# Optimization experiments

Measured on AMD Instinct MI355X. Metric: run time of the kernel, lower is better.

## Reference

```python
import jax, jax.numpy as jnp
import numpy as np

B, D, E, H, O, TOP_K = 65536, 256, 16, 256, 256, 2
GATE_T = 1.0  # gate_temperature default


def setup_inputs() -> dict:
    key = jax.random.key(0)
    ks = jax.random.split(key, 8)
    sn = lambda k, shape, sc: (jax.random.normal(k, shape, jnp.float32) * sc)
    return {
        "x": sn(ks[0], (B, D), 1.0),
        # per-expert input bias, init N(0, 0.02) as in the module
        "bias": sn(ks[1], (E, D), 0.02),
        # expert MLP params: Linear(D,H) -> ReLU -> Linear(H,O), stacked over experts
        "W1": sn(ks[2], (E, D, H), 1.0 / np.sqrt(D)),
        "b1": jnp.zeros((E, H), jnp.float32),
        "W2": sn(ks[3], (E, H, O), 1.0 / np.sqrt(H)),
        "b2": jnp.zeros((E, O), jnp.float32),
        # gate MLP: Linear(D,4D) -> ReLU -> Linear(4D,D) -> ReLU -> Linear(D,E)
        "g1": sn(ks[4], (D, 4 * D), 1.0 / np.sqrt(D)),
        "gb1": jnp.zeros((4 * D,), jnp.float32),
        "g2": sn(ks[5], (4 * D, D), 1.0 / np.sqrt(4 * D)),
        "gb2": jnp.zeros((D,), jnp.float32),
        "g3": sn(ks[6], (D, E), 1.0 / np.sqrt(D)),
        "gb3": jnp.zeros((E,), jnp.float32),
    }


def reference(x, bias, W1, b1, W2, b2, g1, gb1, g2, gb2, g3, gb3):
    # --- gate ---
    h = jax.nn.relu(x @ g1 + gb1)
    h = jax.nn.relu(h @ g2 + gb2)
    gate_logits = h @ g3 + gb3              # [B, E]
    T = max(GATE_T, 1e-6)
    p = jax.nn.softmax(gate_logits / T, axis=1)

    # --- top-k sparsification + renormalize (top_k < num_experts) ---
    topv, topi = jax.lax.top_k(p, TOP_K)    # [B, K]
    rows = jnp.arange(p.shape[0])[:, None]
    p_sparse = jnp.zeros_like(p).at[rows, topi].set(topv)
    p = p_sparse / (p_sparse.sum(axis=1, keepdims=True) + 1e-9)

    # --- dense all-experts compute (module runs every expert on every token) ---
    xb = x[:, None, :] + bias[None]                                  # [B, E, D]
    he = jax.nn.relu(jnp.einsum("bed,edh->beh", xb, W1) + b1)      # [B, E, H]
    outs_all = jnp.einsum("beh,eho->beo", he, W2) + b2             # [B, E, O]

    # --- weighted combine (stopgrad_gate=False -> grads flow through p) ---
    y = jnp.einsum("be,beo->bo", p, outs_all)                      # [B, O]
    return (y, p)
```

## Files before the change

kernel.cpp:

```cpp
#include <hip/hip_runtime.h>
#include <cstdint>
#include <cstddef>

#define BTOK 65536
#define DDIM 256
#define NEXP 16
#define HDIM 256
#define ODIM 256
#define TAU2 1.2e-2f
#define TAU3 1.2e-4
#define AMB2_CAP 12288
#define AMB3_CAP 1024

typedef _Float16 fp16x8 __attribute__((ext_vector_type(8)));
typedef float    f32x4_t __attribute__((ext_vector_type(4)));

__device__ __forceinline__ void async_ld16(const void* g, void* l) {
  __builtin_amdgcn_global_load_lds(
      (const __attribute__((address_space(1))) unsigned int*)g,
      (__attribute__((address_space(3))) unsigned int*)l, 16, 0, 0);
}

__global__ __launch_bounds__(256) void k_transpose_cvt(
    const float* __restrict__ src, _Float16* __restrict__ dhi,
    _Float16* __restrict__ dlo, int R, int C) {
  __shared__ float s[32][33];
  int bz = blockIdx.z;
  size_t stride = (size_t)R * C;
  src += (size_t)bz * stride;
  dhi += (size_t)bz * stride;
  if (dlo) dlo += (size_t)bz * stride;
  int c0 = blockIdx.x * 32, r0 = blockIdx.y * 32;
  int tx = threadIdx.x & 31, ty = threadIdx.x >> 5;
  for (int k = 0; k < 32; k += 8)
    s[ty + k][tx] = src[(size_t)(r0 + ty + k) * C + c0 + tx];
  __syncthreads();
  for (int k = 0; k < 32; k += 8) {
    float v = s[tx][ty + k];
    _Float16 h = (_Float16)v;
    size_t o = (size_t)(c0 + ty + k) * R + r0 + tx;
    dhi[o] = h;
    if (dlo) dlo[o] = (_Float16)(v - (float)h);
  }
}

__global__ __launch_bounds__(256) void k_xcvt_hi(const float* __restrict__ x,
                                                 _Float16* __restrict__ xhi, int n8) {
  int i = blockIdx.x * 256 + threadIdx.x;
  if (i >= n8) return;
  const float4* p = (const float4*)x;
  float4 a = p[(size_t)i * 2], b = p[(size_t)i * 2 + 1];
  float v[8] = {a.x, a.y, a.z, a.w, b.x, b.y, b.z, b.w};
  fp16x8 hv;
#pragma unroll
  for (int j = 0; j < 8; j++) hv[j] = (_Float16)v[j];
  *(fp16x8*)(xhi + (size_t)i * 8) = hv;
}

__global__ __launch_bounds__(256) void k_gemm_f16(
    const _Float16* __restrict__ A, const _Float16* __restrict__ B,
    const float* __restrict__ bias, _Float16* __restrict__ C,
    int M, int N, int K) {
  __shared__ _Float16 sA[128 * 32], sB[128 * 32];
  const int tid = threadIdx.x;
  const int lane = tid & 63;
  const int wave = tid >> 6;
  const int wr = wave >> 1, wc = wave & 1;
  const int m0 = blockIdx.y * 128, n0 = blockIdx.x * 128;
  f32x4_t zero4 = {0.f, 0.f, 0.f, 0.f};
  f32x4_t acc[4][4];
#pragma unroll
  for (int i = 0; i < 4; i++)
#pragma unroll
    for (int j = 0; j < 4; j++) acc[i][j] = zero4;

  for (int k0 = 0; k0 < K; k0 += 32) {
#pragma unroll
    for (int r = 0; r < 2; r++) {
      int idx = r * 256 + tid;
      int row = idx >> 2, ch = idx & 3;
      int gch = ch ^ (row & 3);
      async_ld16(A + (size_t)(m0 + row) * K + k0 + gch * 8, &sA[idx * 8]);
      async_ld16(B + (size_t)(n0 + row) * K + k0 + gch * 8, &sB[idx * 8]);
    }
    __syncthreads();
    fp16x8 a[4], b[4];
    int kc = lane >> 4;
#pragma unroll
    for (int i = 0; i < 4; i++) {
      int ar = wr * 64 + i * 16 + (lane & 15);
      a[i] = *(const fp16x8*)&sA[ar * 32 + ((kc ^ (ar & 3)) << 3)];
      int br = wc * 64 + i * 16 + (lane & 15);
      b[i] = *(const fp16x8*)&sB[br * 32 + ((kc ^ (br & 3)) << 3)];
    }
#pragma unroll
    for (int i = 0; i < 4; i++)
#pragma unroll
      for (int j = 0; j < 4; j++)
        acc[i][j] = __builtin_amdgcn_mfma_f32_16x16x32_f16(a[i], b[j], acc[i][j], 0, 0, 0);
    __syncthreads();
  }
#pragma unroll
  for (int j = 0; j < 4; j++) {
    int col = n0 + wc * 64 + j * 16 + (lane & 15);
    float bc = bias[col];
#pragma unroll
    for (int i = 0; i < 4; i++)
#pragma unroll
      for (int q = 0; q < 4; q++) {
        int row = m0 + wr * 64 + i * 16 + ((lane >> 4) << 2) + q;
        float v = acc[i][j][q] + bc;
        v = v > 0.f ? v : 0.f;
        C[(size_t)row * N + col] = (_Float16)v;
      }
  }
}

__global__ __launch_bounds__(256) void k_gemm_split(
    const _Float16* __restrict__ Ahi, const _Float16* __restrict__ Alo,
    const _Float16* __restrict__ Bhi, const _Float16* __restrict__ Blo,
    const float* __restrict__ bias,
    _Float16* __restrict__ Chi, _Float16* __restrict__ Clo,
    int M, int N, int K, const int* __restrict__ nAct) {
  int nA = *nAct;
  if (nA > M) nA = M;
  const int m0 = blockIdx.y * 128, n0 = blockIdx.x * 128;
  if (m0 >= nA) return;
  __shared__ _Float16 sAh[128 * 32], sAl[128 * 32], sBh[128 * 32], sBl[128 * 32];
  const int tid = threadIdx.x;
  const int lane = tid & 63;
  const int wave = tid >> 6;
  const int wr = wave >> 1, wc = wave & 1;
  f32x4_t zero4 = {0.f, 0.f, 0.f, 0.f};
  f32x4_t acc[4][4];
#pragma unroll
  for (int i = 0; i < 4; i++)
#pragma unroll
    for (int j = 0; j < 4; j++) acc[i][j] = zero4;

  for (int k0 = 0; k0 < K; k0 += 32) {
#pragma unroll
    for (int r = 0; r < 2; r++) {
      int idx = r * 256 + tid;
      int row = idx >> 2, ch = idx & 3;
      int gch = ch ^ (row & 3);
      size_t ga = (size_t)(m0 + row) * K + k0 + gch * 8;
      size_t gb = (size_t)(n0 + row) * K + k0 + gch * 8;
      async_ld16(Ahi + ga, &sAh[idx * 8]);
      async_ld16(Alo + ga, &sAl[idx * 8]);
      async_ld16(Bhi + gb, &sBh[idx * 8]);
      async_ld16(Blo + gb, &sBl[idx * 8]);
    }
    __syncthreads();
    fp16x8 ah[4], al[4], bh[4], bl[4];
    int kc = lane >> 4;
#pragma unroll
    for (int i = 0; i < 4; i++) {
      int ar = wr * 64 + i * 16 + (lane & 15);
      int offa = ar * 32 + ((kc ^ (ar & 3)) << 3);
      ah[i] = *(const fp16x8*)&sAh[offa];
      al[i] = *(const fp16x8*)&sAl[offa];
      int br = wc * 64 + i * 16 + (lane & 15);
      int offb = br * 32 + ((kc ^ (br & 3)) << 3);
      bh[i] = *(const fp16x8*)&sBh[offb];
      bl[i] = *(const fp16x8*)&sBl[offb];
    }
#pragma unroll
    for (int i = 0; i < 4; i++)
#pragma unroll
      for (int j = 0; j < 4; j++) {
        acc[i][j] = __builtin_amdgcn_mfma_f32_16x16x32_f16(ah[i], bh[j], acc[i][j], 0, 0, 0);
        acc[i][j] = __builtin_amdgcn_mfma_f32_16x16x32_f16(ah[i], bl[j], acc[i][j], 0, 0, 0);
        acc[i][j] = __builtin_amdgcn_mfma_f32_16x16x32_f16(al[i], bh[j], acc[i][j], 0, 0, 0);
      }
    __syncthreads();
  }
#pragma unroll
  for (int j = 0; j < 4; j++) {
    int col = n0 + wc * 64 + j * 16 + (lane & 15);
    float bc = bias[col];
#pragma unroll
    for (int i = 0; i < 4; i++)
#pragma unroll
      for (int q = 0; q < 4; q++) {
        int row = m0 + wr * 64 + i * 16 + ((lane >> 4) << 2) + q;
        float v = acc[i][j][q] + bc;
        v = v > 0.f ? v : 0.f;
        _Float16 h = (_Float16)v;
        size_t o = (size_t)row * N + col;
        Chi[o] = h;
        Clo[o] = (_Float16)(v - (float)h);
      }
  }
}

__global__ __launch_bounds__(256) void k_gate3_fast(
    const _Float16* __restrict__ h2h, const float* __restrict__ g3,
    const float* __restrict__ gb3,
    float* __restrict__ pout, int* __restrict__ idx0, int* __restrict__ idx1,
    float* __restrict__ w0, float* __restrict__ w1,
    int* __restrict__ amb2Cnt, int* __restrict__ amb2List,
    int* __restrict__ cnt0, int* __restrict__ cnt1) {
  __shared__ _Float16 shh[16 * 256];
  __shared__ float sg3[16][260];
  __shared__ float sgb[16];
  __shared__ float slog[16][17];
  __shared__ int sidx[16][2];
  __shared__ float swv[16][2];
  __shared__ int hc0[16], hc1[16];
  int tid = threadIdx.x;
  int tokBase = blockIdx.x * 16;
  if (tid < 16) { hc0[tid] = 0; hc1[tid] = 0; }
  {
    int t = tid >> 4, c = (tid & 15) * 16;
    size_t g = (size_t)(tokBase + t) * 256 + c;
    *(fp16x8*)&shh[t * 256 + c] = *(const fp16x8*)&h2h[g];
    *(fp16x8*)&shh[t * 256 + c + 8] = *(const fp16x8*)&h2h[g + 8];
  }
#pragma unroll
  for (int r = 0; r < 16; r++) {
    int j = r * 256 + tid;
    sg3[j & 15][j >> 4] = g3[j];
  }
  if (tid < 16) sgb[tid] = gb3[tid];
  __syncthreads();
  int t = tid >> 4, e = tid & 15;
  const _Float16* ph = &shh[t * 256];
  const float* pg = &sg3[e][0];
  float acc = 0.f;
  for (int k = 0; k < 256; k += 8) {
    fp16x8 hv = *(const fp16x8*)&ph[k];
    float4 ga = *(const float4*)&pg[k];
    float4 gb = *(const float4*)&pg[k + 4];
    acc = fmaf((float)hv[0], ga.x, acc);
    acc = fmaf((float)hv[1], ga.y, acc);
    acc = fmaf((float)hv[2], ga.z, acc);
    acc = fmaf((float)hv[3], ga.w, acc);
    acc = fmaf((float)hv[4], gb.x, acc);
    acc = fmaf((float)hv[5], gb.y, acc);
    acc = fmaf((float)hv[6], gb.z, acc);
    acc = fmaf((float)hv[7], gb.w, acc);
  }
  acc += sgb[e];
  slog[t][e] = acc;
  __syncthreads();
  if (e == 0) {
    float l[16];
#pragma unroll
    for (int i = 0; i < 16; i++) l[i] = slog[t][i];
    int i1 = 0;
    for (int i = 1; i < 16; i++) if (l[i] > l[i1]) i1 = i;
    int i2 = -1;
    for (int i = 0; i < 16; i++) { if (i == i1) continue; if (i2 < 0 || l[i] > l[i2]) i2 = i; }
    float l3 = -1e30f;
    for (int i = 0; i < 16; i++) { if (i == i1 || i == i2) continue; if (l[i] > l3) l3 = l[i]; }
    float lmax = l[i1];
    float S = 0.f;
    for (int i = 0; i < 16; i++) S += expf(l[i] - lmax);
    float p1 = 1.0f / S, p2 = expf(l[i2] - lmax) / S;
    float den = p1 + p2 + 1e-9f;
    sidx[t][0] = i1; sidx[t][1] = i2;
    swv[t][0] = p1 / den; swv[t][1] = p2 / den;
    atomicAdd(&hc0[i1], 1);
    atomicAdd(&hc1[i2], 1);
    if (l[i2] - l3 < TAU2) {
      int pos = atomicAdd(amb2Cnt, 1);
      if (pos < AMB2_CAP) amb2List[pos] = tokBase + t;
    }
  }
  __syncthreads();
  int i1 = sidx[t][0], i2 = sidx[t][1];
  float pv = (e == i1) ? swv[t][0] : ((e == i2) ? swv[t][1] : 0.f);
  pout[(size_t)(tokBase + t) * 16 + e] = pv;
  if (e == 0) {
    int tok = tokBase + t;
    idx0[tok] = i1; idx1[tok] = i2;
    w0[tok] = swv[t][0]; w1[tok] = swv[t][1];
  }
  if (tid < 16) {
    if (hc0[tid]) atomicAdd(&cnt0[tid], hc0[tid]);
    if (hc1[tid]) atomicAdd(&cnt1[tid], hc1[tid]);
  }
}

__global__ __launch_bounds__(256) void k_gather2(
    const float* __restrict__ x, const int* __restrict__ cnt,
    const int* __restrict__ list,
    _Float16* __restrict__ xgh, _Float16* __restrict__ xgl) {
  int n = *cnt; if (n > AMB2_CAP) n = AMB2_CAP;
  int s = blockIdx.x * 8 + (threadIdx.x >> 5);
  if (s >= n) return;
  int tok = list[s];
  int c = (threadIdx.x & 31) * 8;
  const float4* p = (const float4*)&x[(size_t)tok * 256 + c];
  float4 a = p[0], b = p[1];
  float v[8] = {a.x, a.y, a.z, a.w, b.x, b.y, b.z, b.w};
  fp16x8 hv, lv;
#pragma unroll
  for (int j = 0; j < 8; j++) {
    _Float16 h = (_Float16)v[j];
    hv[j] = h;
    lv[j] = (_Float16)(v[j] - (float)h);
  }
  *(fp16x8*)&xgh[(size_t)s * 256 + c] = hv;
  *(fp16x8*)&xgl[(size_t)s * 256 + c] = lv;
}

__global__ __launch_bounds__(256) void k_gate3_precise(
    const _Float16* __restrict__ h2ghi, const _Float16* __restrict__ h2glo,
    const float* __restrict__ g3, const float* __restrict__ gb3,
    const int* __restrict__ amb2Cnt, const int* __restrict__ amb2List,
    float* __restrict__ pout, int* __restrict__ idx0, int* __restrict__ idx1,
    float* __restrict__ w0, float* __restrict__ w1,
    int* __restrict__ amb3Cnt, int* __restrict__ amb3List,
    int* __restrict__ cnt0, int* __restrict__ cnt1) {
  __shared__ _Float16 shh[16 * 256], shl[16 * 256];
  __shared__ float sg3[16][260];
  __shared__ float sgb[16];
  __shared__ double slog[16][17];
  __shared__ int sidx[16][2];
  __shared__ float swv[16][2];
  int tid = threadIdx.x;
  int slotBase = blockIdx.x * 16;
  int n2 = *amb2Cnt; if (n2 > AMB2_CAP) n2 = AMB2_CAP;
  {
    int t = tid >> 4, c = (tid & 15) * 16;
    size_t g = (size_t)(slotBase + t) * 256 + c;
    *(fp16x8*)&shh[t * 256 + c] = *(const fp16x8*)&h2ghi[g];
    *(fp16x8*)&shh[t * 256 + c + 8] = *(const fp16x8*)&h2ghi[g + 8];
    *(fp16x8*)&shl[t * 256 + c] = *(const fp16x8*)&h2glo[g];
    *(fp16x8*)&shl[t * 256 + c + 8] = *(const fp16x8*)&h2glo[g + 8];
  }
#pragma unroll
  for (int r = 0; r < 16; r++) {
    int j = r * 256 + tid;
    sg3[j & 15][j >> 4] = g3[j];
  }
  if (tid < 16) sgb[tid] = gb3[tid];
  __syncthreads();
  int t = tid >> 4, e = tid & 15;
  int slot = slotBase + t;
  const _Float16* ph = &shh[t * 256];
  const _Float16* pl = &shl[t * 256];
  const float* pg = &sg3[e][0];
  double acc = 0.0;
  for (int k = 0; k < 256; k += 4) {
#pragma unroll
    for (int j = 0; j < 4; j++) {
      double a = (double)(float)ph[k + j] + (double)(float)pl[k + j];
      acc = fma(a, (double)pg[k + j], acc);
    }
  }
  acc += (double)sgb[e];
  slog[t][e] = acc;
  __syncthreads();
  if (e == 0 && slot < n2) {
    int tok = amb2List[slot];
    double l[16];
#pragma unroll
    for (int i = 0; i < 16; i++) l[i] = slog[t][i];
    int i1 = 0;
    for (int i = 1; i < 16; i++) if (l[i] > l[i1]) i1 = i;
    int i2 = -1;
    for (int i = 0; i < 16; i++) { if (i == i1) continue; if (i2 < 0 || l[i] > l[i2]) i2 = i; }
    double l3 = -1e300;
    for (int i = 0; i < 16; i++) { if (i == i1 || i == i2) continue; if (l[i] > l3) l3 = l[i]; }
    double lmax = l[i1];
    double S = 0.0;
    for (int i = 0; i < 16; i++) S += exp(l[i] - lmax);
    double p1 = 1.0 / S, p2 = exp(l[i2] - lmax) / S;
    double den = p1 + p2 + 1e-9;
    sidx[t][0] = i1; sidx[t][1] = i2;
    swv[t][0] = (float)(p1 / den); swv[t][1] = (float)(p2 / den);
    int o0 = idx0[tok], o1 = idx1[tok];
    if (i1 != o0) { atomicSub(&cnt0[o0], 1); atomicAdd(&cnt0[i1], 1); }
    if (i2 != o1) { atomicSub(&cnt1[o1], 1); atomicAdd(&cnt1[i2], 1); }
    if (l[i2] - l3 < TAU3) {
      int pos = atomicAdd(amb3Cnt, 1);
      if (pos < AMB3_CAP) amb3List[pos] = tok;
    }
  }
  __syncthreads();
  if (slot < n2) {
    int tok = amb2List[slot];
    int i1 = sidx[t][0], i2 = sidx[t][1];
    float pv = (e == i1) ? swv[t][0] : ((e == i2) ? swv[t][1] : 0.f);
    pout[(size_t)tok * 16 + e] = pv;
    if (e == 0) {
      idx0[tok] = i1; idx1[tok] = i2;
      w0[tok] = swv[t][0]; w1[tok] = swv[t][1];
    }
  }
}

__global__ __launch_bounds__(256) void k_ref_l1(
    const float* __restrict__ x, const float* __restrict__ g1,
    const float* __restrict__ gb1,
    const int* __restrict__ cnt, const int* __restrict__ list,
    double* __restrict__ h1d) {
  int n = *cnt; if (n > AMB3_CAP) n = AMB3_CAP;
  int t = blockIdx.y;
  if (t >= n) return;
  __shared__ float sx[256];
  __shared__ double sred[4][64];
  int tid = threadIdx.x;
  int tok = list[t];
  sx[tid] = x[(size_t)tok * 256 + tid];
  __syncthreads();
  int o = tid & 63, p = tid >> 6;
  int out = blockIdx.x * 64 + o;
  double a = 0.0;
  const float* gp = g1 + (size_t)(p * 64) * 1024 + out;
  const float* xp = &sx[p * 64];
#pragma unroll 8
  for (int k = 0; k < 64; k++)
    a = fma((double)xp[k], (double)gp[(size_t)k * 1024], a);
  sred[p][o] = a;
  __syncthreads();
  if (p == 0) {
    double s = sred[0][o] + sred[1][o] + sred[2][o] + sred[3][o] + (double)gb1[out];
    h1d[(size_t)t * 1024 + out] = s > 0.0 ? s : 0.0;
  }
}

__global__ __launch_bounds__(512) void k_ref_l2(
    const double* __restrict__ h1d, const float* __restrict__ g2,
    const float* __restrict__ gb2,
    const int* __restrict__ cnt, double* __restrict__ h2d) {
  int n = *cnt; if (n > AMB3_CAP) n = AMB3_CAP;
  int t = blockIdx.y;
  if (t >= n) return;
  __shared__ double sh1[1024];
  __shared__ double sred[8][64];
  int tid = threadIdx.x;
  sh1[tid] = h1d[(size_t)t * 1024 + tid];
  sh1[512 + tid] = h1d[(size_t)t * 1024 + 512 + tid];
  __syncthreads();
  int o = tid & 63, p = tid >> 6;
  int out = blockIdx.x * 64 + o;
  double a = 0.0;
  const float* gp = g2 + (size_t)(p * 128) * 256 + out;
  const double* hp = &sh1[p * 128];
#pragma unroll 4
  for (int k = 0; k < 128; k++)
    a = fma(hp[k], (double)gp[(size_t)k * 256], a);
  sred[p][o] = a;
  __syncthreads();
  if (p == 0) {
    double s = sred[0][o] + sred[1][o] + sred[2][o] + sred[3][o] +
               sred[4][o] + sred[5][o] + sred[6][o] + sred[7][o] + (double)gb2[out];
    h2d[(size_t)t * 256 + out] = s > 0.0 ? s : 0.0;
  }
}

__global__ __launch_bounds__(256) void k_ref_l3(
    const double* __restrict__ h2d, const float* __restrict__ g3,
    const float* __restrict__ gb3,
    const int* __restrict__ cnt, const int* __restrict__ list,
    float* __restrict__ pout, int* __restrict__ idx0, int* __restrict__ idx1,
    float* __restrict__ w0, float* __restrict__ w1,
    int* __restrict__ cnt0, int* __restrict__ cnt1) {
  int n = *cnt; if (n > AMB3_CAP) n = AMB3_CAP;
  int t = blockIdx.x;
  if (t >= n) return;
  __shared__ double sh2[256];
  __shared__ double sl16[16][17];
  __shared__ int sidx[2];
  __shared__ float swv[2];
  int tid = threadIdx.x;
  int tok = list[t];
  sh2[tid] = h2d[(size_t)t * 256 + tid];
  __syncthreads();
  {
    int o = tid & 15, pp = tid >> 4;
    double a = 0.0;
#pragma unroll
    for (int k = pp * 16; k < pp * 16 + 16; k++)
      a = fma(sh2[k], (double)g3[(size_t)k * 16 + o], a);
    sl16[pp][o] = a;
  }
  __syncthreads();
  if (tid == 0) {
    double l[16];
    for (int o = 0; o < 16; o++) {
      double a = (double)gb3[o];
      for (int p = 0; p < 16; p++) a += sl16[p][o];
      l[o] = a;
    }
    int i1 = 0;
    for (int i = 1; i < 16; i++) if (l[i] > l[i1]) i1 = i;
    int i2 = -1;
    for (int i = 0; i < 16; i++) { if (i == i1) continue; if (i2 < 0 || l[i] > l[i2]) i2 = i; }
    double lmax = l[i1];
    double S = 0.0;
    for (int i = 0; i < 16; i++) S += exp(l[i] - lmax);
    double p1 = 1.0 / S, p2 = exp(l[i2] - lmax) / S;
    double den = p1 + p2 + 1e-9;
    float fw0 = (float)(p1 / den), fw1 = (float)(p2 / den);
    int o0 = idx0[tok], o1 = idx1[tok];
    if (i1 != o0) { atomicSub(&cnt0[o0], 1); atomicAdd(&cnt0[i1], 1); }
    if (i2 != o1) { atomicSub(&cnt1[o1], 1); atomicAdd(&cnt1[i2], 1); }
    sidx[0] = i1; sidx[1] = i2;
    swv[0] = fw0; swv[1] = fw1;
    idx0[tok] = i1; idx1[tok] = i2;
    w0[tok] = fw0; w1[tok] = fw1;
  }
  __syncthreads();
  if (tid < 16) {
    float pv = (tid == sidx[0]) ? swv[0] : ((tid == sidx[1]) ? swv[1] : 0.f);
    pout[(size_t)tok * 16 + tid] = pv;
  }
}

__global__ void k_offsets(const int* __restrict__ cnt0, const int* __restrict__ cnt1,
                          int* off0, int* off1, int* cur0, int* cur1,
                          int* dExp0, int* dRow0, int* dExp1, int* dRow1, int* nTiles) {
  if (threadIdx.x == 0) {
    int tot = 0, nt = 0;
    for (int e = 0; e < 16; e++) {
      off0[e] = tot; cur0[e] = 0;
      int tiles = (cnt0[e] + 127) >> 7;
      for (int ti = 0; ti < tiles; ti++) { dExp0[nt] = e; dRow0[nt] = tot + ti * 128; nt++; }
      tot += tiles * 128;
    }
    nTiles[0] = nt;
    tot = 0; nt = 0;
    for (int e = 0; e < 16; e++) {
      off1[e] = tot; cur1[e] = 0;
      int tiles = (cnt1[e] + 127) >> 7;
      for (int ti = 0; ti < tiles; ti++) { dExp1[nt] = e; dRow1[nt] = tot + ti * 128; nt++; }
      tot += tiles * 128;
    }
    nTiles[1] = nt;
  }
}

__global__ __launch_bounds__(256) void k_scatter(
    const int* __restrict__ idx0, const int* __restrict__ idx1,
    const float* __restrict__ w0, const float* __restrict__ w1,
    const int* __restrict__ off0, const int* __restrict__ off1,
    int* cur0, int* cur1,
    int* __restrict__ tok0, float* __restrict__ wl0,
    int* __restrict__ tok1, float* __restrict__ wl1) {
  __shared__ int c0[16], c1[16], b0[16], b1[16];
  int tid = threadIdx.x;
  if (tid < 16) { c0[tid] = 0; c1[tid] = 0; }
  __syncthreads();
  int b = blockIdx.x * 256 + tid;
  int e0 = idx0[b], e1 = idx1[b];
  int r0 = atomicAdd(&c0[e0], 1);
  int r1 = atomicAdd(&c1[e1], 1);
  __syncthreads();
  if (tid < 16) { b0[tid] = atomicAdd(&cur0[tid], c0[tid]); b1[tid] = atomicAdd(&cur1[tid], c1[tid]); }
  __syncthreads();
  int p0 = off0[e0] + b0[e0] + r0;
  tok0[p0] = b; wl0[p0] = w0[b];
  int p1 = off1[e1] + b1[e1] + r1;
  tok1[p1] = b; wl1[p1] = w1[b];
}

template <int PASSB>
__global__ __launch_bounds__(512) void k_expert(
    const _Float16* __restrict__ xhi, const float* __restrict__ bias,
    const _Float16* __restrict__ W1T, const float* __restrict__ b1,
    const _Float16* __restrict__ W2T, const float* __restrict__ b2,
    const int* __restrict__ dExp, const int* __restrict__ dRow,
    const int* __restrict__ nT,
    const int* __restrict__ tokL, const float* __restrict__ wL,
    float* __restrict__ y) {
  __shared__ _Float16 sA[128 * 64];
  __shared__ _Float16 sB[256 * 64];
  __shared__ _Float16 sHE[128 * 264];
  __shared__ int sTok[128];
  __shared__ float sW[128];
  int tid = threadIdx.x, lane = tid & 63, wave = tid >> 6;
  int wr = wave >> 2, wc = wave & 3;
  f32x4_t zero4 = {0.f, 0.f, 0.f, 0.f};
  int nt = *nT;
  for (int t = blockIdx.x; t < nt; t += gridDim.x) {
    int e = dExp[t], rowOff = dRow[t];
    if (tid < 128) { sTok[tid] = tokL[rowOff + tid]; sW[tid] = wL[rowOff + tid]; }
    __syncthreads();
    f32x4_t acc[4][4];
#pragma unroll
    for (int i = 0; i < 4; i++)
#pragma unroll
      for (int j = 0; j < 4; j++) acc[i][j] = zero4;
    const _Float16* W1e = W1T + (size_t)e * 65536;
    const _Float16* W2e = W2T + (size_t)e * 65536;
    const float* be = bias + e * 256;
    for (int k0 = 0; k0 < 256; k0 += 64) {
#pragma unroll
      for (int r = 0; r < 2; r++) {
        int idx = r * 512 + tid;
        int row = idx >> 3, ch = idx & 7, gch = ch ^ (row & 7);
        int tok = sTok[row];
        int tk = tok < 0 ? 0 : tok;
        fp16x8 v = *(const fp16x8*)&xhi[(size_t)tk * 256 + k0 + gch * 8];
        const float* bp = &be[k0 + gch * 8];
#pragma unroll
        for (int j = 0; j < 8; j++) v[j] = (_Float16)((float)v[j] + bp[j]);
        *(fp16x8*)&sA[row * 64 + ch * 8] = v;
      }
#pragma unroll
      for (int r = 0; r < 4; r++) {
        int idx = r * 512 + tid;
        int row = idx >> 3, ch = idx & 7, gch = ch ^ (row & 7);
        *(fp16x8*)&sB[row * 64 + ch * 8] =
            *(const fp16x8*)&W1e[(size_t)row * 256 + k0 + gch * 8];
      }
      __syncthreads();
#pragma unroll
      for (int kk = 0; kk < 2; kk++) {
        fp16x8 a[4], bf[4];
        int kcg = kk * 4 + (lane >> 4);
#pragma unroll
        for (int i = 0; i < 4; i++) {
          int ar = wr * 64 + i * 16 + (lane & 15);
          a[i] = *(const fp16x8*)&sA[ar * 64 + (kcg ^ (ar & 7)) * 8];
          int br = wc * 64 + i * 16 + (lane & 15);
          bf[i] = *(const fp16x8*)&sB[br * 64 + (kcg ^ (br & 7)) * 8];
        }
#pragma unroll
        for (int i = 0; i < 4; i++)
#pragma unroll
          for (int j = 0; j < 4; j++)
            acc[i][j] = __builtin_amdgcn_mfma_f32_16x16x32_f16(a[i], bf[j], acc[i][j], 0, 0, 0);
      }
      __syncthreads();
    }
#pragma unroll
    for (int j = 0; j < 4; j++) {
      int col = wc * 64 + j * 16 + (lane & 15);
      float bb = b1[e * 256 + col];
#pragma unroll
      for (int i = 0; i < 4; i++)
#pragma unroll
        for (int q = 0; q < 4; q++) {
          int row = wr * 64 + i * 16 + ((lane >> 4) << 2) + q;
          float v = acc[i][j][q] + bb;
          v = v > 0.f ? v : 0.f;
          sHE[row * 264 + col] = (_Float16)v;
        }
    }
#pragma unroll
    for (int i = 0; i < 4; i++)
#pragma unroll
      for (int j = 0; j < 4; j++) acc[i][j] = zero4;
    __syncthreads();
    for (int k0 = 0; k0 < 256; k0 += 64) {
#pragma unroll
      for (int r = 0; r < 4; r++) {
        int idx = r * 512 + tid;
        int row = idx >> 3, ch = idx & 7, gch = ch ^ (row & 7);
        *(fp16x8*)&sB[row * 64 + ch * 8] =
            *(const fp16x8*)&W2e[(size_t)row * 256 + k0 + gch * 8];
      }
      __syncthreads();
#pragma unroll
      for (int kk = 0; kk < 2; kk++) {
        fp16x8 a[4], bf[4];
        int kcg = kk * 4 + (lane >> 4);
#pragma unroll
        for (int i = 0; i < 4; i++) {
          int ar = wr * 64 + i * 16 + (lane & 15);
          a[i] = *(const fp16x8*)&sHE[ar * 264 + k0 + kk * 32 + (lane >> 4) * 8];
          int br = wc * 64 + i * 16 + (lane & 15);
          bf[i] = *(const fp16x8*)&sB[br * 64 + (kcg ^ (br & 7)) * 8];
        }
#pragma unroll
        for (int i = 0; i < 4; i++)
#pragma unroll
          for (int j = 0; j < 4; j++)
            acc[i][j] = __builtin_amdgcn_mfma_f32_16x16x32_f16(a[i], bf[j], acc[i][j], 0, 0, 0);
      }
      __syncthreads();
    }
#pragma unroll
    for (int j = 0; j < 4; j++) {
      int col = wc * 64 + j * 16 + (lane & 15);
      float bb = b2[e * 256 + col];
#pragma unroll
      for (int i = 0; i < 4; i++)
#pragma unroll
        for (int q = 0; q < 4; q++) {
          int row = wr * 64 + i * 16 + ((lane >> 4) << 2) + q;
          int tok = sTok[row];
          if (tok >= 0) {
            float v = (acc[i][j][q] + bb) * sW[row];
            size_t o = (size_t)tok * 256 + col;
            if (PASSB) y[o] += v; else y[o] = v;
          }
        }
    }
    __syncthreads();
  }
}

extern "C" void kernel_launch(void* const* d_in, const int* in_sizes, int n_in,
                              void* d_out, int out_size, void* d_ws, size_t ws_size,
                              hipStream_t stream) {
  const float* x   = (const float*)d_in[0];
  const float* bias= (const float*)d_in[1];
  const float* W1  = (const float*)d_in[2];
  const float* b1  = (const float*)d_in[3];
  const float* W2  = (const float*)d_in[4];
  const float* b2  = (const float*)d_in[5];
  const float* g1  = (const float*)d_in[6];
  const float* gb1 = (const float*)d_in[7];
  const float* g2  = (const float*)d_in[8];
  const float* gb2 = (const float*)d_in[9];
  const float* g3  = (const float*)d_in[10];
  const float* gb3 = (const float*)d_in[11];
  float* y    = (float*)d_out;
  float* pout = y + (size_t)BTOK * 256;

  char* w = (char*)d_ws;
  auto alloc = [&](size_t bytes) -> char* {
    char* p = w;
    w += (bytes + 255) & ~(size_t)255;
    return p;
  };
  _Float16* xhi  = (_Float16*)alloc((size_t)BTOK * 256 * 2);
  _Float16* h2h  = (_Float16*)alloc((size_t)BTOK * 256 * 2);
  _Float16* g1Th = (_Float16*)alloc((size_t)256 * 1024 * 2);
  _Float16* g1Tl = (_Float16*)alloc((size_t)256 * 1024 * 2);
  _Float16* g2Th = (_Float16*)alloc((size_t)256 * 1024 * 2);
  _Float16* g2Tl = (_Float16*)alloc((size_t)256 * 1024 * 2);
  _Float16* W1T  = (_Float16*)alloc((size_t)16 * 65536 * 2);
  _Float16* W2T  = (_Float16*)alloc((size_t)16 * 65536 * 2);
  int*   idx0 = (int*)alloc((size_t)BTOK * 4);
  int*   idx1 = (int*)alloc((size_t)BTOK * 4);
  float* w0a  = (float*)alloc((size_t)BTOK * 4);
  float* w1a  = (float*)alloc((size_t)BTOK * 4);
  int*   ctrl = (int*)alloc(4096);
  int*   amb2List = (int*)alloc((size_t)AMB2_CAP * 4);
  int*   amb3List = (int*)alloc((size_t)AMB3_CAP * 4);
  int*   dExp0 = (int*)alloc(544 * 4);
  int*   dRow0 = (int*)alloc(544 * 4);
  int*   dExp1 = (int*)alloc(544 * 4);
  int*   dRow1 = (int*)alloc(544 * 4);
  const int LCAP = BTOK + 16 * 128;
  int*   tok0 = (int*)alloc((size_t)LCAP * 4);
  float* wl0  = (float*)alloc((size_t)LCAP * 4);
  int*   tok1 = (int*)alloc((size_t)LCAP * 4);
  float* wl1  = (float*)alloc((size_t)LCAP * 4);
  _Float16* xgh  = (_Float16*)alloc((size_t)AMB2_CAP * 256 * 2);
  _Float16* xgl  = (_Float16*)alloc((size_t)AMB2_CAP * 256 * 2);
  _Float16* h1gh = (_Float16*)alloc((size_t)AMB2_CAP * 1024 * 2);
  _Float16* h1gl = (_Float16*)alloc((size_t)AMB2_CAP * 1024 * 2);
  _Float16* h2gh = (_Float16*)alloc((size_t)AMB2_CAP * 256 * 2);
  _Float16* h2gl = (_Float16*)alloc((size_t)AMB2_CAP * 256 * 2);
  double* h1d = (double*)alloc((size_t)AMB3_CAP * 1024 * 8);
  double* h2d = (double*)alloc((size_t)AMB3_CAP * 256 * 8);

  size_t used = (size_t)(w - (char*)d_ws);
  size_t remain = ws_size > used ? ws_size - used : 0;
  int CG = 1;
  while (CG < 64 && (size_t)(BTOK / CG) * 1024 * 2 + 1024 > remain) CG <<= 1;
  int MC = BTOK / CG;
  _Float16* h1h = (_Float16*)alloc((size_t)MC * 1024 * 2);

  int* cnt0 = ctrl + 0;  int* cnt1 = ctrl + 16;
  int* off0 = ctrl + 32; int* off1 = ctrl + 48;
  int* cur0 = ctrl + 64; int* cur1 = ctrl + 80;
  int* nTiles = ctrl + 96;
  int* amb2Cnt = ctrl + 112;
  int* amb3Cnt = ctrl + 116;

  hipMemsetAsync(ctrl, 0, 4096, stream);
  hipMemsetAsync(tok0, 0xFF, (size_t)LCAP * 4, stream);
  hipMemsetAsync(tok1, 0xFF, (size_t)LCAP * 4, stream);

  dim3 tb(256);
  k_transpose_cvt<<<dim3(32, 8, 1), tb, 0, stream>>>(g1, g1Th, g1Tl, 256, 1024);
  k_transpose_cvt<<<dim3(8, 32, 1), tb, 0, stream>>>(g2, g2Th, g2Tl, 1024, 256);
  k_transpose_cvt<<<dim3(8, 8, 16), tb, 0, stream>>>(W1, W1T, nullptr, 256, 256);
  k_transpose_cvt<<<dim3(8, 8, 16), tb, 0, stream>>>(W2, W2T, nullptr, 256, 256);
  k_xcvt_hi<<<(BTOK * 256 / 8 + 255) / 256, tb, 0, stream>>>(x, xhi, BTOK * 256 / 8);

  for (int c = 0; c < CG; c++) {
    const _Float16* xh = xhi + (size_t)c * MC * 256;
    k_gemm_f16<<<dim3(8, MC / 128), tb, 0, stream>>>(xh, g1Th, gb1, h1h, MC, 1024, 256);
    k_gemm_f16<<<dim3(2, MC / 128), tb, 0, stream>>>(h1h, g2Th, gb2,
                                                     h2h + (size_t)c * MC * 256, MC, 256, 1024);
  }
  k_gate3_fast<<<BTOK / 16, tb, 0, stream>>>(h2h, g3, gb3, pout, idx0, idx1,
                                             w0a, w1a, amb2Cnt, amb2List, cnt0, cnt1);

  k_gather2<<<AMB2_CAP / 8, tb, 0, stream>>>(x, amb2Cnt, amb2List, xgh, xgl);
  k_gemm_split<<<dim3(8, AMB2_CAP / 128), tb, 0, stream>>>(
      xgh, xgl, g1Th, g1Tl, gb1, h1gh, h1gl, AMB2_CAP, 1024, 256, amb2Cnt);
  k_gemm_split<<<dim3(2, AMB2_CAP / 128), tb, 0, stream>>>(
      h1gh, h1gl, g2Th, g2Tl, gb2, h2gh, h2gl, AMB2_CAP, 256, 1024, amb2Cnt);
  k_gate3_precise<<<AMB2_CAP / 16, tb, 0, stream>>>(
      h2gh, h2gl, g3, gb3, amb2Cnt, amb2List, pout, idx0, idx1, w0a, w1a,
      amb3Cnt, amb3List, cnt0, cnt1);

  k_ref_l1<<<dim3(16, AMB3_CAP), tb, 0, stream>>>(x, g1, gb1, amb3Cnt, amb3List, h1d);
  k_ref_l2<<<dim3(4, AMB3_CAP), 512, 0, stream>>>(h1d, g2, gb2, amb3Cnt, h2d);
  k_ref_l3<<<AMB3_CAP, tb, 0, stream>>>(h2d, g3, gb3, amb3Cnt, amb3List,
                                        pout, idx0, idx1, w0a, w1a, cnt0, cnt1);

  k_offsets<<<1, 64, 0, stream>>>(cnt0, cnt1, off0, off1, cur0, cur1,
                                  dExp0, dRow0, dExp1, dRow1, nTiles);
  k_scatter<<<BTOK / 256, tb, 0, stream>>>(idx0, idx1, w0a, w1a, off0, off1,
                                           cur0, cur1, tok0, wl0, tok1, wl1);
  k_expert<0><<<528, 512, 0, stream>>>(xhi, bias, W1T, b1, W2T, b2,
                                       dExp0, dRow0, nTiles + 0, tok0, wl0, y);
  k_expert<1><<<528, 512, 0, stream>>>(xhi, bias, W1T, b1, W2T, b2,
                                       dExp1, dRow1, nTiles + 1, tok1, wl1, y);
}
```

Before: 686.0 us.

## Split expert MLP into batched layer-1 and layer-2 grouped GEMM kernels

```diff
diff --git a/kernel.cpp b/kernel.cpp
--- a/kernel.cpp
+++ b/kernel.cpp
@@ -11,6 +11,7 @@
 #define TAU3 1.2e-4
 #define AMB2_CAP 12288
 #define AMB3_CAP 1024
+#define LCAP (BTOK + 2048)
 
 typedef _Float16 fp16x8 __attribute__((ext_vector_type(8)));
 typedef float    f32x4_t __attribute__((ext_vector_type(4)));
@@ -514,21 +515,21 @@
 
 __global__ void k_offsets(const int* __restrict__ cnt0, const int* __restrict__ cnt1,
                           int* off0, int* off1, int* cur0, int* cur1,
-                          int* dExp0, int* dRow0, int* dExp1, int* dRow1, int* nTiles) {
+                          int* dExpC, int* dRowC, int* nTiles) {
   if (threadIdx.x == 0) {
     int tot = 0, nt = 0;
     for (int e = 0; e < 16; e++) {
       off0[e] = tot; cur0[e] = 0;
       int tiles = (cnt0[e] + 127) >> 7;
-      for (int ti = 0; ti < tiles; ti++) { dExp0[nt] = e; dRow0[nt] = tot + ti * 128; nt++; }
+      for (int ti = 0; ti < tiles; ti++) { dExpC[nt] = e; dRowC[nt] = tot + ti * 128; nt++; }
       tot += tiles * 128;
     }
     nTiles[0] = nt;
-    tot = 0; nt = 0;
+    tot = 0;
     for (int e = 0; e < 16; e++) {
       off1[e] = tot; cur1[e] = 0;
       int tiles = (cnt1[e] + 127) >> 7;
-      for (int ti = 0; ti < tiles; ti++) { dExp1[nt] = e; dRow1[nt] = tot + ti * 128; nt++; }
+      for (int ti = 0; ti < tiles; ti++) { dExpC[nt] = e; dRowC[nt] = LCAP + tot + ti * 128; nt++; }
       tot += tiles * 128;
     }
     nTiles[1] = nt;
@@ -559,27 +560,24 @@
   tok1[p1] = b; wl1[p1] = w1[b];
 }
 
-template <int PASSB>
-__global__ __launch_bounds__(512) void k_expert(
+__global__ __launch_bounds__(512) void k_grp_l1(
     const _Float16* __restrict__ xhi, const float* __restrict__ bias,
     const _Float16* __restrict__ W1T, const float* __restrict__ b1,
-    const _Float16* __restrict__ W2T, const float* __restrict__ b2,
+    const int* __restrict__ tokAll,
     const int* __restrict__ dExp, const int* __restrict__ dRow,
-    const int* __restrict__ nT,
-    const int* __restrict__ tokL, const float* __restrict__ wL,
-    float* __restrict__ y) {
-  __shared__ _Float16 sA[128 * 64];
-  __shared__ _Float16 sB[256 * 64];
-  __shared__ _Float16 sHE[128 * 264];
+    const int* __restrict__ nT, _Float16* __restrict__ heg) {
+  __shared__ _Float16 sA[128 * 32];
+  __shared__ _Float16 sB[256 * 32];
   __shared__ int sTok[128];
-  __shared__ float sW[128];
+  __shared__ float sBias[256];
   int tid = threadIdx.x, lane = tid & 63, wave = tid >> 6;
   int wr = wave >> 2, wc = wave & 3;
   f32x4_t zero4 = {0.f, 0.f, 0.f, 0.f};
   int nt = *nT;
   for (int t = blockIdx.x; t < nt; t += gridDim.x) {
     int e = dExp[t], rowOff = dRow[t];
-    if (tid < 128) { sTok[tid] = tokL[rowOff + tid]; sW[tid] = wL[rowOff + tid]; }
+    if (tid < 128) sTok[tid] = tokAll[rowOff + tid];
+    if (tid < 256) sBias[tid] = bias[e * 256 + tid];
     __syncthreads();
     f32x4_t acc[4][4];
 #pragma unroll
@@ -587,46 +585,38 @@
 #pragma unroll
       for (int j = 0; j < 4; j++) acc[i][j] = zero4;
     const _Float16* W1e = W1T + (size_t)e * 65536;
-    const _Float16* W2e = W2T + (size_t)e * 65536;
-    const float* be = bias + e * 256;
-    for (int k0 = 0; k0 < 256; k0 += 64) {
-#pragma unroll
-      for (int r = 0; r < 2; r++) {
-        int idx = r * 512 + tid;
-        int row = idx >> 3, ch = idx & 7, gch = ch ^ (row & 7);
+    for (int k0 = 0; k0 < 256; k0 += 32) {
+      {
+        int row = tid >> 2, ch = tid & 3, gch = ch ^ (row & 3);
         int tok = sTok[row];
         int tk = tok < 0 ? 0 : tok;
         fp16x8 v = *(const fp16x8*)&xhi[(size_t)tk * 256 + k0 + gch * 8];
-        const float* bp = &be[k0 + gch * 8];
+        const float* bp = &sBias[k0 + gch * 8];
 #pragma unroll
         for (int j = 0; j < 8; j++) v[j] = (_Float16)((float)v[j] + bp[j]);
-        *(fp16x8*)&sA[row * 64 + ch * 8] = v;
+        *(fp16x8*)&sA[tid * 8] = v;
       }
 #pragma unroll
-      for (int r = 0; r < 4; r++) {
+      for (int r = 0; r < 2; r++) {
         int idx = r * 512 + tid;
-        int row = idx >> 3, ch = idx & 7, gch = ch ^ (row & 7);
-        *(fp16x8*)&sB[row * 64 + ch * 8] =
-            *(const fp16x8*)&W1e[(size_t)row * 256 + k0 + gch * 8];
+        int row = idx >> 2, ch = idx & 3, gch = ch ^ (row & 3);
+        async_ld16(W1e + (size_t)row * 256 + k0 + gch * 8, &sB[idx * 8]);
       }
       __syncthreads();
-#pragma unroll
-      for (int kk = 0; kk < 2; kk++) {
-        fp16x8 a[4], bf[4];
-        int kcg = kk * 4 + (lane >> 4);
-#pragma unroll
-        for (int i = 0; i < 4; i++) {
-          int ar = wr * 64 + i * 16 + (lane & 15);
-          a[i] = *(const fp16x8*)&sA[ar * 64 + (kcg ^ (ar & 7)) * 8];
-          int br = wc * 64 + i * 16 + (lane & 15);
-          bf[i] = *(const fp16x8*)&sB[br * 64 + (kcg ^ (br & 7)) * 8];
-        }
-#pragma unroll
-        for (int i = 0; i < 4; i++)
-#pragma unroll
-          for (int j = 0; j < 4; j++)
-            acc[i][j] = __builtin_amdgcn_mfma_f32_16x16x32_f16(a[i], bf[j], acc[i][j], 0, 0, 0);
+      fp16x8 a[4], b[4];
+      int kc = lane >> 4;
+#pragma unroll
+      for (int i = 0; i < 4; i++) {
+        int ar = wr * 64 + i * 16 + (lane & 15);
+        a[i] = *(const fp16x8*)&sA[ar * 32 + ((kc ^ (ar & 3)) << 3)];
+        int br = wc * 64 + i * 16 + (lane & 15);
+        b[i] = *(const fp16x8*)&sB[br * 32 + ((kc ^ (br & 3)) << 3)];
       }
+#pragma unroll
+      for (int i = 0; i < 4; i++)
+#pragma unroll
+        for (int j = 0; j < 4; j++)
+          acc[i][j] = __builtin_amdgcn_mfma_f32_16x16x32_f16(a[i], b[j], acc[i][j], 0, 0, 0);
       __syncthreads();
     }
 #pragma unroll
@@ -639,41 +629,66 @@
         for (int q = 0; q < 4; q++) {
           int row = wr * 64 + i * 16 + ((lane >> 4) << 2) + q;
           float v = acc[i][j][q] + bb;
-          v = v > 0.f ? v : 0.f;
-          sHE[row * 264 + col] = (_Float16)v;
+          heg[(size_t)(rowOff + row) * 256 + col] = (_Float16)(v > 0.f ? v : 0.f);
         }
     }
+    __syncthreads();
+  }
+}
+
+template <int PASSB>
+__global__ __launch_bounds__(512) void k_grp_l2(
+    const _Float16* __restrict__ heg, const _Float16* __restrict__ W2T,
+    const float* __restrict__ b2,
+    const int* __restrict__ tokAll, const float* __restrict__ wlAll,
+    const int* __restrict__ dExp, const int* __restrict__ dRow,
+    const int* __restrict__ nT0, const int* __restrict__ nTC,
+    float* __restrict__ y) {
+  __shared__ _Float16 sA[128 * 32];
+  __shared__ _Float16 sB[256 * 32];
+  __shared__ int sTok[128];
+  __shared__ float sW[128];
+  int tid = threadIdx.x, lane = tid & 63, wave = tid >> 6;
+  int wr = wave >> 2, wc = wave & 3;
+  f32x4_t zero4 = {0.f, 0.f, 0.f, 0.f};
+  int tStart = PASSB ? *nT0 : 0;
+  int tEnd = PASSB ? *nTC : *nT0;
+  for (int t = tStart + blockIdx.x; t < tEnd; t += gridDim.x) {
+    int e = dExp[t], rowOff = dRow[t];
+    if (tid < 128) { sTok[tid] = tokAll[rowOff + tid]; sW[tid] = wlAll[rowOff + tid]; }
+    __syncthreads();
+    f32x4_t acc[4][4];
 #pragma unroll
     for (int i = 0; i < 4; i++)
 #pragma unroll
       for (int j = 0; j < 4; j++) acc[i][j] = zero4;
-    __syncthreads();
-    for (int k0 = 0; k0 < 256; k0 += 64) {
-#pragma unroll
-      for (int r = 0; r < 4; r++) {
+    const _Float16* W2e = W2T + (size_t)e * 65536;
+    for (int k0 = 0; k0 < 256; k0 += 32) {
+      {
+        int row = tid >> 2, ch = tid & 3, gch = ch ^ (row & 3);
+        async_ld16(heg + (size_t)(rowOff + row) * 256 + k0 + gch * 8, &sA[tid * 8]);
+      }
+#pragma unroll
+      for (int r = 0; r < 2; r++) {
         int idx = r * 512 + tid;
-        int row = idx >> 3, ch = idx & 7, gch = ch ^ (row & 7);
-        *(fp16x8*)&sB[row * 64 + ch * 8] =
-            *(const fp16x8*)&W2e[(size_t)row * 256 + k0 + gch * 8];
+        int row = idx >> 2, ch = idx & 3, gch = ch ^ (row & 3);
+        async_ld16(W2e + (size_t)row * 256 + k0 + gch * 8, &sB[idx * 8]);
       }
       __syncthreads();
-#pragma unroll
-      for (int kk = 0; kk < 2; kk++) {
-        fp16x8 a[4], bf[4];
-        int kcg = kk * 4 + (lane >> 4);
-#pragma unroll
-        for (int i = 0; i < 4; i++) {
-          int ar = wr * 64 + i * 16 + (lane & 15);
-          a[i] = *(const fp16x8*)&sHE[ar * 264 + k0 + kk * 32 + (lane >> 4) * 8];
-          int br = wc * 64 + i * 16 + (lane & 15);
-          bf[i] = *(const fp16x8*)&sB[br * 64 + (kcg ^ (br & 7)) * 8];
-        }
-#pragma unroll
-        for (int i = 0; i < 4; i++)
-#pragma unroll
-          for (int j = 0; j < 4; j++)
-            acc[i][j] = __builtin_amdgcn_mfma_f32_16x16x32_f16(a[i], bf[j], acc[i][j], 0, 0, 0);
+      fp16x8 a[4], b[4];
+      int kc = lane >> 4;
+#pragma unroll
+      for (int i = 0; i < 4; i++) {
+        int ar = wr * 64 + i * 16 + (lane & 15);
+        a[i] = *(const fp16x8*)&sA[ar * 32 + ((kc ^ (ar & 3)) << 3)];
+        int br = wc * 64 + i * 16 + (lane & 15);
+        b[i] = *(const fp16x8*)&sB[br * 32 + ((kc ^ (br & 3)) << 3)];
       }
+#pragma unroll
+      for (int i = 0; i < 4; i++)
+#pragma unroll
+        for (int j = 0; j < 4; j++)
+          acc[i][j] = __builtin_amdgcn_mfma_f32_16x16x32_f16(a[i], b[j], acc[i][j], 0, 0, 0);
       __syncthreads();
     }
 #pragma unroll
@@ -736,21 +751,17 @@
   int*   ctrl = (int*)alloc(4096);
   int*   amb2List = (int*)alloc((size_t)AMB2_CAP * 4);
   int*   amb3List = (int*)alloc((size_t)AMB3_CAP * 4);
-  int*   dExp0 = (int*)alloc(544 * 4);
-  int*   dRow0 = (int*)alloc(544 * 4);
-  int*   dExp1 = (int*)alloc(544 * 4);
-  int*   dRow1 = (int*)alloc(544 * 4);
-  const int LCAP = BTOK + 16 * 128;
-  int*   tok0 = (int*)alloc((size_t)LCAP * 4);
-  float* wl0  = (float*)alloc((size_t)LCAP * 4);
-  int*   tok1 = (int*)alloc((size_t)LCAP * 4);
-  float* wl1  = (float*)alloc((size_t)LCAP * 4);
+  int*   dExpC = (int*)alloc(1088 * 4);
+  int*   dRowC = (int*)alloc(1088 * 4);
+  int*   tokAll = (int*)alloc((size_t)2 * LCAP * 4);
+  float* wlAll  = (float*)alloc((size_t)2 * LCAP * 4);
   _Float16* xgh  = (_Float16*)alloc((size_t)AMB2_CAP * 256 * 2);
   _Float16* xgl  = (_Float16*)alloc((size_t)AMB2_CAP * 256 * 2);
   _Float16* h1gh = (_Float16*)alloc((size_t)AMB2_CAP * 1024 * 2);
   _Float16* h1gl = (_Float16*)alloc((size_t)AMB2_CAP * 1024 * 2);
   _Float16* h2gh = (_Float16*)alloc((size_t)AMB2_CAP * 256 * 2);
   _Float16* h2gl = (_Float16*)alloc((size_t)AMB2_CAP * 256 * 2);
+  _Float16* heg = (_Float16*)xgh;
   double* h1d = (double*)alloc((size_t)AMB3_CAP * 1024 * 8);
   double* h2d = (double*)alloc((size_t)AMB3_CAP * 256 * 8);
 
@@ -769,8 +780,7 @@
   int* amb3Cnt = ctrl + 116;
 
   hipMemsetAsync(ctrl, 0, 4096, stream);
-  hipMemsetAsync(tok0, 0xFF, (size_t)LCAP * 4, stream);
-  hipMemsetAsync(tok1, 0xFF, (size_t)LCAP * 4, stream);
+  hipMemsetAsync(tokAll, 0xFF, (size_t)2 * LCAP * 4, stream);
 
   dim3 tb(256);
   k_transpose_cvt<<<dim3(32, 8, 1), tb, 0, stream>>>(g1, g1Th, g1Tl, 256, 1024);
@@ -803,11 +813,14 @@
                                         pout, idx0, idx1, w0a, w1a, cnt0, cnt1);
 
   k_offsets<<<1, 64, 0, stream>>>(cnt0, cnt1, off0, off1, cur0, cur1,
-                                  dExp0, dRow0, dExp1, dRow1, nTiles);
+                                  dExpC, dRowC, nTiles);
   k_scatter<<<BTOK / 256, tb, 0, stream>>>(idx0, idx1, w0a, w1a, off0, off1,
-                                           cur0, cur1, tok0, wl0, tok1, wl1);
-  k_expert<0><<<528, 512, 0, stream>>>(xhi, bias, W1T, b1, W2T, b2,
-                                       dExp0, dRow0, nTiles + 0, tok0, wl0, y);
-  k_expert<1><<<528, 512, 0, stream>>>(xhi, bias, W1T, b1, W2T, b2,
-                                       dExp1, dRow1, nTiles + 1, tok1, wl1, y);
-}
+                                           cur0, cur1, tokAll, wlAll,
+                                           tokAll + LCAP, wlAll + LCAP);
+  k_grp_l1<<<1056, 512, 0, stream>>>(xhi, bias, W1T, b1, tokAll,
+                                     dExpC, dRowC, nTiles + 1, heg);
+  k_grp_l2<0><<<528, 512, 0, stream>>>(heg, W2T, b2, tokAll, wlAll,
+                                       dExpC, dRowC, nTiles, nTiles + 1, y);
+  k_grp_l2<1><<<528, 512, 0, stream>>>(heg, W2T, b2, tokAll, wlAll,
+                                       dExpC, dRowC, nTiles, nTiles + 1, y);
+}
```

New measurement: 726.8 us. 1.06x slower.
